# Optimization experiments

Hardware: AMD Instinct MI355X
Metric: run time of the kernel (lower is better)

The kernel has to match this reference:

```python
import jax, jax.numpy as jnp
import numpy as np

B, L, H, NH, NB = 16, 256, 64, 2, 2
HS = H // NH
MAXLEN, TIME_SPAN, ITEMNUM = 256, 256, 50000
NEG = -4294967295.0  # -2**32 + 1
EPS = 1e-8


def layernorm(x, g, b):
    m = jnp.mean(x, axis=-1, keepdims=True)
    v = jnp.mean((x - m) ** 2, axis=-1, keepdims=True)
    return g * (x - m) / jnp.sqrt(v + EPS) + b


def setup_inputs() -> dict:
    key = jax.random.key(0)
    ks = jax.random.split(key, 24)
    s = 0.02
    inp = {
        "seqs_data": jax.random.randint(ks[0], (B, L), 0, ITEMNUM, dtype=jnp.int32),
        "seqs": jax.random.normal(ks[1], (B, L, H), dtype=jnp.float32),
        "positions": jax.random.randint(ks[2], (B, L), 0, MAXLEN, dtype=jnp.int32),
        "time_matrices": jax.random.randint(ks[3], (B, L, L), 0, TIME_SPAN + 1, dtype=jnp.int32),
        "abs_pos_K_tab": jax.random.normal(ks[4], (MAXLEN, H)) * s,
        "abs_pos_V_tab": jax.random.normal(ks[5], (MAXLEN, H)) * s,
        "time_K_tab": jax.random.normal(ks[6], (TIME_SPAN + 1, H)) * s,
        "time_V_tab": jax.random.normal(ks[7], (TIME_SPAN + 1, H)) * s,
        "Qw": jax.random.normal(ks[8], (NB, H, H)) * s,
        "Qb": jnp.zeros((NB, H)),
        "Kw": jax.random.normal(ks[9], (NB, H, H)) * s,
        "Kb": jnp.zeros((NB, H)),
        "Vw": jax.random.normal(ks[10], (NB, H, H)) * s,
        "Vb": jnp.zeros((NB, H)),
        "ln1_g": jnp.ones((NB, H)), "ln1_b": jnp.zeros((NB, H)),
        "ln2_g": jnp.ones((NB, H)), "ln2_b": jnp.zeros((NB, H)),
        "ffn_W1": jax.random.normal(ks[11], (NB, H, H)) * s,
        "ffn_b1": jnp.zeros((NB, H)),
        "ffn_W2": jax.random.normal(ks[12], (NB, H, H)) * s,
        "ffn_b2": jnp.zeros((NB, H)),
        "last_g": jnp.ones((H,)), "last_b": jnp.zeros((H,)),
    }
    return inp


def _forward(seqs_data, seqs, positions, time_matrices,
             abs_pos_K_tab, abs_pos_V_tab, time_K_tab, time_V_tab,
             Qw, Qb, Kw, Kb, Vw, Vb, ln1_g, ln1_b, ln2_g, ln2_b,
             ffn_W1, ffn_b1, ffn_W2, ffn_b2, last_g, last_b):
    # abs-pos embeddings with padding_idx=0 (zero row, no grad flow to it)
    pos_keep = (positions != 0)[..., None].astype(seqs.dtype)
    abs_pos_K = abs_pos_K_tab[positions] * pos_keep            # [B,L,H]
    abs_pos_V = abs_pos_V_tab[positions] * pos_keep
    time_K = time_K_tab[time_matrices]                         # [B,L,L,H]
    time_V = time_V_tab[time_matrices]
    tmK = time_K.reshape(B, L, L, NH, HS)
    tmV = time_V.reshape(B, L, L, NH, HS)
    aK = abs_pos_K.reshape(B, L, NH, HS)
    aV = abs_pos_V.reshape(B, L, NH, HS)

    timeline_mask = (seqs_data == ITEMNUM - 1)                 # [B,L] True = pad
    keep = (~timeline_mask)[..., None].astype(seqs.dtype)
    seqs = seqs * keep
    causal = ~jnp.tril(jnp.ones((L, L), dtype=bool))           # [L,L] upper tri
    full_mask = timeline_mask[:, None, :, None] | causal[None, None]  # [B,1,L,L]

    for i in range(NB):
        q_in = layernorm(seqs, ln1_g[i], ln1_b[i])
        Q = (q_in @ Qw[i].T + Qb[i]).reshape(B, L, NH, HS)
        K = (seqs @ Kw[i].T + Kb[i]).reshape(B, L, NH, HS)
        V = (seqs @ Vw[i].T + Vb[i]).reshape(B, L, NH, HS)
        aw = (jnp.einsum('blhd,bmhd->bhlm', Q, K)
              + jnp.einsum('blhd,bmhd->bhlm', Q, aK)
              + jnp.einsum('blmhd,blhd->bhlm', tmK, Q)) / (HS ** 0.5)
        aw = jnp.where(full_mask, NEG, aw)
        A = jax.nn.softmax(aw, axis=-1)                        # [B,NH,L,L]
        out = (jnp.einsum('bhlm,bmhd->blhd', A, V)
               + jnp.einsum('bhlm,bmhd->blhd', A, aV)
               + jnp.einsum('bhlm,blmhd->blhd', A, tmV)).reshape(B, L, H)
        seqs = q_in + out
        seqs = layernorm(seqs, ln2_g[i], ln2_b[i])
        h = jax.nn.relu(seqs @ ffn_W1[i].T + ffn_b1[i])
        seqs = (h @ ffn_W2[i].T + ffn_b2[i]) + seqs
        seqs = seqs * keep
    return layernorm(seqs, last_g, last_b)


def reference(seqs_data, seqs, positions, time_matrices,
              abs_pos_K_tab, abs_pos_V_tab, time_K_tab, time_V_tab,
              Qw, Qb, Kw, Kb, Vw, Vb, ln1_g, ln1_b, ln2_g, ln2_b,
              ffn_W1, ffn_b1, ffn_W2, ffn_b2, last_g, last_b):
    return _forward(seqs_data, seqs, positions, time_matrices,
                    abs_pos_K_tab, abs_pos_V_tab, time_K_tab, time_V_tab,
                    Qw, Qb, Kw, Kb, Vw, Vb, ln1_g, ln1_b, ln2_g, ln2_b,
                    ffn_W1, ffn_b1, ffn_W2, ffn_b2, last_g, last_b)
```

## Files before the change

### kernel.cpp

```cpp
#include <hip/hip_runtime.h>
#include <math.h>

#define SEQL  256
#define HDIM  64
#define PADID 49999
#define NEGV  -4294967295.0f
#define LNEPS 1e-8f
#define INV_SQRT_HS 0.17677669529663687f
#define TKC   257
#define TKTLD 260
#define QG    4
#define ROWS  4096

struct AttnS {
    float qs[QG][HDIM];
    float Tk[QG][2][TKTLD];
    float A[QG][2][SEQL];
    float Wl[QG][2][TKTLD];
    float outred[4][QG][HDIM];
    float redm[QG][2][4];
    float reds[QG][2][4];
};
struct WorkS {
    float t0[64][65];
    float t1[64][65];
    float xs[4][HDIM];
    float qs[4][HDIM];
    float kx[HDIM][5];
};
union SmemU { AttnS a; WorkS w; };

struct FArgs {
    const int *seqs_data, *positions, *tmat;
    const float *apK, *apV, *tVtab, *tKtabT;
    const float *Qo_in, *KpT_in, *Vp_in, *q_in_in;
    const float *g2, *b2, *W1, *fb1, *W2, *fb2;
    const float *g1n, *b1n, *Qw, *Qb, *Kw, *Kb, *Vw, *Vb;
    float *q_in_out, *Qo_out, *KpT_out, *Vp_out;
    const float *lastg, *lastb;
    float *out;
    int final_ln;
};

__device__ __forceinline__ float waveReduceSum(float v) {
#pragma unroll
    for (int o = 32; o > 0; o >>= 1) v += __shfl_xor(v, o);
    return v;
}

__global__ __launch_bounds__(256, 4) void prep_kernel(
    const float* __restrict__ seqs, const int* __restrict__ seqs_data,
    const int* __restrict__ positions,
    const float* __restrict__ Qw, const float* __restrict__ Qb,
    const float* __restrict__ Kw, const float* __restrict__ Kb,
    const float* __restrict__ Vw, const float* __restrict__ Vb,
    const float* __restrict__ g1, const float* __restrict__ b1,
    const float* __restrict__ apK, const float* __restrict__ apV,
    const float* __restrict__ tKtab, float* __restrict__ tKtabT,
    float* __restrict__ q_in, float* __restrict__ Qo,
    float* __restrict__ KpT, float* __restrict__ Vp)
{
    __shared__ WorkS sw;
    const int tid = threadIdx.x;
    const int hw = blockIdx.x;
    const int blk = ((hw & 7) << 7) | (hw >> 3);
    const int w = tid >> 6, t = tid & 63;
    const int row0 = blk << 2;
    const int row = row0 + w;

    if (hw < 5) {
        const int s0 = hw * 64;
        const int nrows = (hw == 4) ? (TKC - 256) : 64;
#pragma unroll
        for (int pp = 0; pp < 16; ++pp) {
            int r = pp*4 + w;
            if (r < nrows) sw.t0[r][t] = tKtab[(size_t)(s0 + r)*64 + t];
        }
        __syncthreads();
#pragma unroll
        for (int pp = 0; pp < 16; ++pp) {
            int dd = pp*4 + w;
            if (t < nrows) tKtabT[dd*TKTLD + s0 + t] = sw.t0[t][dd];
        }
        __syncthreads();
    }

    float x = seqs[(size_t)row * HDIM + t];
    if (seqs_data[row] == PADID) x = 0.f;
    float mean = waveReduceSum(x) * (1.f / HDIM);
    float d = x - mean;
    float var = waveReduceSum(d * d) * (1.f / HDIM);
    float q = g1[t] * d / sqrtf(var + LNEPS) + b1[t];

    sw.xs[w][t] = x;
    sw.qs[w][t] = q;
    q_in[(size_t)row * HDIM + t] = q;

    int pos = positions[row];
    float aK = pos ? apK[(size_t)pos * HDIM + t] : 0.f;
    float aV = pos ? apV[(size_t)pos * HDIM + t] : 0.f;

#pragma unroll
    for (int pp = 0; pp < 16; ++pp) {
        sw.t0[pp*4 + w][t] = Qw[(size_t)(pp*4 + w)*64 + t];
        sw.t1[pp*4 + w][t] = Kw[(size_t)(pp*4 + w)*64 + t];
    }
    __syncthreads();
    float aq = 0.f, ak = 0.f;
#pragma unroll 16
    for (int mth = 0; mth < 64; ++mth) {
        aq += sw.qs[w][mth] * sw.t0[t][mth];
        ak += sw.xs[w][mth] * sw.t1[t][mth];
    }
    Qo[(size_t)row*HDIM + t] = aq + Qb[t];
    sw.kx[t][w] = ak + Kb[t] + aK;
    __syncthreads();
#pragma unroll
    for (int pp = 0; pp < 16; ++pp)
        sw.t0[pp*4 + w][t] = Vw[(size_t)(pp*4 + w)*64 + t];
    KpT[(size_t)(tid>>2)*ROWS + row0 + (tid&3)] = sw.kx[tid>>2][tid&3];
    __syncthreads();
    float av = 0.f;
#pragma unroll 16
    for (int mth = 0; mth < 64; ++mth)
        av += sw.xs[w][mth] * sw.t0[t][mth];
    Vp[(size_t)row*HDIM + t] = av + Vb[t] + aV;
}

__global__ __launch_bounds__(256, 4) void attn_ffn_kernel(FArgs p)
{
    __shared__ SmemU sm;
    __shared__ float x2s[QG][HDIM];
    const int tid = threadIdx.x;
    const int hw = blockIdx.x;
    const int blk = ((hw & 7) << 7) | (hw >> 3);
    const int b = blk >> 6, al0 = (blk & 63) << 2;
    const int row0 = blk << 2;
    const int w = tid >> 6, t = tid & 63;
    const int m = tid, lane = t, wv = w;

    for (int k = tid; k < QG*2*TKTLD; k += 256) (&sm.a.Wl[0][0][0])[k] = 0.f;
    sm.a.qs[w][t] = p.Qo_in[(size_t)(row0 + w)*HDIM + t];
    bool qpad[QG]; bool anypad = false;
#pragma unroll
    for (int li = 0; li < QG; ++li) {
        qpad[li] = (p.seqs_data[row0 + li] == PADID);
        anypad |= qpad[li];
    }
    const int lmax = al0 + QG - 1;
    int tmc[QG];
#pragma unroll
    for (int li = 0; li < QG; ++li)
        tmc[li] = p.tmat[(size_t)(row0 + li)*SEQL + m];
    __syncthreads();

    for (int c = tid; c < TKC; c += 256) {
        float a00=0,a10=0,a20=0,a30=0,a01=0,a11=0,a21=0,a31=0;
#pragma unroll 8
        for (int dd = 0; dd < 32; ++dd) {
            float tt = p.tKtabT[dd*TKTLD + c];
            a00 += tt*sm.a.qs[0][dd]; a10 += tt*sm.a.qs[1][dd];
            a20 += tt*sm.a.qs[2][dd]; a30 += tt*sm.a.qs[3][dd];
        }
#pragma unroll 8
        for (int dd = 32; dd < 64; ++dd) {
            float tt = p.tKtabT[dd*TKTLD + c];
            a01 += tt*sm.a.qs[0][dd]; a11 += tt*sm.a.qs[1][dd];
            a21 += tt*sm.a.qs[2][dd]; a31 += tt*sm.a.qs[3][dd];
        }
        sm.a.Tk[0][0][c]=a00; sm.a.Tk[1][0][c]=a10; sm.a.Tk[2][0][c]=a20; sm.a.Tk[3][0][c]=a30;
        sm.a.Tk[0][1][c]=a01; sm.a.Tk[1][1][c]=a11; sm.a.Tk[2][1][c]=a21; sm.a.Tk[3][1][c]=a31;
    }
    __syncthreads();

    float p0v[QG], p1v[QG];
    const bool waveAllMasked = (wv*64 > lmax) && !anypad;
    if (waveAllMasked) {
#pragma unroll
        for (int li = 0; li < QG; ++li) { p0v[li] = NEGV; p1v[li] = NEGV; }
    } else {
        float s0[QG] = {0,0,0,0}, s1[QG] = {0,0,0,0};
        const float* kpb = p.KpT_in + (size_t)b*SEQL + m;
#pragma unroll 8
        for (int dd = 0; dd < 32; ++dd) {
            float kv0 = kpb[(size_t)dd*ROWS];
            float kv1 = kpb[(size_t)(dd+32)*ROWS];
#pragma unroll
            for (int li = 0; li < QG; ++li) {
                s0[li] += kv0 * sm.a.qs[li][dd];
                s1[li] += kv1 * sm.a.qs[li][dd+32];
            }
        }
#pragma unroll
        for (int li = 0; li < QG; ++li) {
            float v0 = (s0[li] + sm.a.Tk[li][0][tmc[li]]) * INV_SQRT_HS;
            float v1 = (s1[li] + sm.a.Tk[li][1][tmc[li]]) * INV_SQRT_HS;
            bool masked = (m > al0 + li) || qpad[li];
            p0v[li] = masked ? NEGV : v0;
            p1v[li] = masked ? NEGV : v1;
        }
    }
#pragma unroll
    for (int li = 0; li < QG; ++li) {
        float a0 = p0v[li], a1 = p1v[li];
#pragma unroll
        for (int o = 32; o > 0; o >>= 1) {
            a0 = fmaxf(a0, __shfl_xor(a0, o));
            a1 = fmaxf(a1, __shfl_xor(a1, o));
        }
        if (lane == 0) { sm.a.redm[li][0][wv] = a0; sm.a.redm[li][1][wv] = a1; }
    }
    __syncthreads();
#pragma unroll
    for (int li = 0; li < QG; ++li) {
        float m0 = fmaxf(fmaxf(sm.a.redm[li][0][0], sm.a.redm[li][0][1]),
                         fmaxf(sm.a.redm[li][0][2], sm.a.redm[li][0][3]));
        float m1 = fmaxf(fmaxf(sm.a.redm[li][1][0], sm.a.redm[li][1][1]),
                         fmaxf(sm.a.redm[li][1][2], sm.a.redm[li][1][3]));
        float e0 = __expf(p0v[li] - m0), e1 = __expf(p1v[li] - m1);
        p0v[li] = e0; p1v[li] = e1;
        float ts0 = waveReduceSum(e0), ts1 = waveReduceSum(e1);
        if (lane == 0) { sm.a.reds[li][0][wv] = ts0; sm.a.reds[li][1][wv] = ts1; }
    }
    __syncthreads();
#pragma unroll
    for (int li = 0; li < QG; ++li) {
        float sum0 = sm.a.reds[li][0][0]+sm.a.reds[li][0][1]+sm.a.reds[li][0][2]+sm.a.reds[li][0][3];
        float sum1 = sm.a.reds[li][1][0]+sm.a.reds[li][1][1]+sm.a.reds[li][1][2]+sm.a.reds[li][1][3];
        float a0 = p0v[li]/sum0, a1 = p1v[li]/sum1;
        sm.a.A[li][0][m] = a0; sm.a.A[li][1][m] = a1;
        if (a0 != 0.f) atomicAdd(&sm.a.Wl[li][0][tmc[li]], a0);
        if (a1 != 0.f) atomicAdd(&sm.a.Wl[li][1][tmc[li]], a1);
    }
    __syncthreads();

    {
        const int hd = lane, chunk = wv, hh = hd >> 5;
        float acc0=0.f, acc1=0.f, acc2=0.f, acc3=0.f;
        const int mend = anypad ? SEQL : (lmax + 1 < SEQL ? lmax + 1 : SEQL);
        const float* vpb = p.Vp_in + (size_t)(b*SEQL)*HDIM + hd;
        int mm = chunk;
        for (; mm + 12 < mend; mm += 16) {
            float v0 = vpb[(size_t)(mm)    * HDIM];
            float v1 = vpb[(size_t)(mm+4)  * HDIM];
            float v2 = vpb[(size_t)(mm+8)  * HDIM];
            float v3 = vpb[(size_t)(mm+12) * HDIM];
            acc0 += sm.a.A[0][hh][mm]*v0 + sm.a.A[0][hh][mm+4]*v1 + sm.a.A[0][hh][mm+8]*v2 + sm.a.A[0][hh][mm+12]*v3;
            acc1 += sm.a.A[1][hh][mm]*v0 + sm.a.A[1][hh][mm+4]*v1 + sm.a.A[1][hh][mm+8]*v2 + sm.a.A[1][hh][mm+12]*v3;
            acc2 += sm.a.A[2][hh][mm]*v0 + sm.a.A[2][hh][mm+4]*v1 + sm.a.A[2][hh][mm+8]*v2 + sm.a.A[2][hh][mm+12]*v3;
            acc3 += sm.a.A[3][hh][mm]*v0 + sm.a.A[3][hh][mm+4]*v1 + sm.a.A[3][hh][mm+8]*v2 + sm.a.A[3][hh][mm+12]*v3;
        }
        for (; mm < mend; mm += 4) {
            float vp = vpb[(size_t)mm * HDIM];
            acc0 += sm.a.A[0][hh][mm]*vp; acc1 += sm.a.A[1][hh][mm]*vp;
            acc2 += sm.a.A[2][hh][mm]*vp; acc3 += sm.a.A[3][hh][mm]*vp;
        }
        const float* tvb = p.tVtab + hd;
        int c = chunk;
        for (; c + 12 < TKC; c += 16) {
            float t0 = tvb[(size_t)(c)    * HDIM];
            float t1 = tvb[(size_t)(c+4)  * HDIM];
            float t2 = tvb[(size_t)(c+8)  * HDIM];
            float t3 = tvb[(size_t)(c+12) * HDIM];
            acc0 += sm.a.Wl[0][hh][c]*t0 + sm.a.Wl[0][hh][c+4]*t1 + sm.a.Wl[0][hh][c+8]*t2 + sm.a.Wl[0][hh][c+12]*t3;
            acc1 += sm.a.Wl[1][hh][c]*t0 + sm.a.Wl[1][hh][c+4]*t1 + sm.a.Wl[1][hh][c+8]*t2 + sm.a.Wl[1][hh][c+12]*t3;
            acc2 += sm.a.Wl[2][hh][c]*t0 + sm.a.Wl[2][hh][c+4]*t1 + sm.a.Wl[2][hh][c+8]*t2 + sm.a.Wl[2][hh][c+12]*t3;
            acc3 += sm.a.Wl[3][hh][c]*t0 + sm.a.Wl[3][hh][c+4]*t1 + sm.a.Wl[3][hh][c+8]*t2 + sm.a.Wl[3][hh][c+12]*t3;
        }
        for (; c < TKC; c += 4) {
            float tv = tvb[(size_t)c * HDIM];
            acc0 += sm.a.Wl[0][hh][c]*tv; acc1 += sm.a.Wl[1][hh][c]*tv;
            acc2 += sm.a.Wl[2][hh][c]*tv; acc3 += sm.a.Wl[3][hh][c]*tv;
        }
        sm.a.outred[chunk][0][hd] = acc0;
        sm.a.outred[chunk][1][hd] = acc1;
        sm.a.outred[chunk][2][hd] = acc2;
        sm.a.outred[chunk][3][hd] = acc3;
    }
    __syncthreads();
    {
        float o = sm.a.outred[0][w][t] + sm.a.outred[1][w][t]
                + sm.a.outred[2][w][t] + sm.a.outred[3][w][t];
        x2s[w][t] = p.q_in_in[(size_t)(row0 + w)*HDIM + t] + o;
    }
    __syncthreads();

    const int row = row0 + w;
    float xv = x2s[w][t];
    float mean = waveReduceSum(xv) * (1.f/HDIM);
    float d = xv - mean;
    float var = waveReduceSum(d*d) * (1.f/HDIM);
    float s = p.g2[t] * d / sqrtf(var + LNEPS) + p.b2[t];
    sm.w.xs[w][t] = s;
#pragma unroll
    for (int pp = 0; pp < 16; ++pp) {
        sm.w.t0[pp*4 + w][t] = p.W1[(size_t)(pp*4 + w)*64 + t];
        sm.w.t1[pp*4 + w][t] = p.W2[(size_t)(pp*4 + w)*64 + t];
    }
    __syncthreads();
    float ha = 0.f;
#pragma unroll 16
    for (int mth = 0; mth < 64; ++mth) ha += sm.w.xs[w][mth] * sm.w.t0[t][mth];
    float hv = fmaxf(ha + p.fb1[t], 0.f);
    sm.w.qs[w][t] = hv;
    float ya = 0.f;
#pragma unroll 16
    for (int mth = 0; mth < 64; ++mth) ya += sm.w.qs[w][mth] * sm.w.t1[t][mth];
    float y = ya + p.fb2[t] + s;
    if (p.seqs_data[row] == PADID) y = 0.f;

    if (!p.final_ln) {
        float mean2 = waveReduceSum(y) * (1.f/HDIM);
        float d2 = y - mean2;
        float var2 = waveReduceSum(d2*d2) * (1.f/HDIM);
        float q = p.g1n[t] * d2 / sqrtf(var2 + LNEPS) + p.b1n[t];
        __syncthreads();
        sm.w.xs[w][t] = y;
        sm.w.qs[w][t] = q;
        p.q_in_out[(size_t)row*HDIM + t] = q;

        int pos = p.positions[row];
        float aK = pos ? p.apK[(size_t)pos*HDIM + t] : 0.f;
        float aV = pos ? p.apV[(size_t)pos*HDIM + t] : 0.f;
#pragma unroll
        for (int pp = 0; pp < 16; ++pp) {
            sm.w.t0[pp*4 + w][t] = p.Qw[(size_t)(pp*4 + w)*64 + t];
            sm.w.t1[pp*4 + w][t] = p.Kw[(size_t)(pp*4 + w)*64 + t];
        }
        __syncthreads();
        float aq = 0.f, ak = 0.f;
#pragma unroll 16
        for (int mth = 0; mth < 64; ++mth) {
            aq += sm.w.qs[w][mth] * sm.w.t0[t][mth];
            ak += sm.w.xs[w][mth] * sm.w.t1[t][mth];
        }
        p.Qo_out[(size_t)row*HDIM + t] = aq + p.Qb[t];
        sm.w.kx[t][w] = ak + p.Kb[t] + aK;
        __syncthreads();
#pragma unroll
        for (int pp = 0; pp < 16; ++pp)
            sm.w.t0[pp*4 + w][t] = p.Vw[(size_t)(pp*4 + w)*64 + t];
        p.KpT_out[(size_t)(tid>>2)*ROWS + row0 + (tid&3)] = sm.w.kx[tid>>2][tid&3];
        __syncthreads();
        float av = 0.f;
#pragma unroll 16
        for (int mth = 0; mth < 64; ++mth)
            av += sm.w.xs[w][mth] * sm.w.t0[t][mth];
        p.Vp_out[(size_t)row*HDIM + t] = av + p.Vb[t] + aV;
    } else {
        float m2 = waveReduceSum(y) * (1.f/HDIM);
        float dd = y - m2;
        float v2 = waveReduceSum(dd*dd) * (1.f/HDIM);
        p.out[(size_t)row*HDIM + t] = p.lastg[t] * dd / sqrtf(v2 + LNEPS) + p.lastb[t];
    }
}

extern "C" void kernel_launch(void* const* d_in, const int* in_sizes, int n_in,
                              void* d_out, int out_size, void* d_ws, size_t ws_size,
                              hipStream_t stream) {
    const int*   seqs_data = (const int*)d_in[0];
    const float* seqs      = (const float*)d_in[1];
    const int*   positions = (const int*)d_in[2];
    const int*   tmat      = (const int*)d_in[3];
    const float* apK       = (const float*)d_in[4];
    const float* apV       = (const float*)d_in[5];
    const float* tKtab     = (const float*)d_in[6];
    const float* tVtab     = (const float*)d_in[7];
    const float* Qw = (const float*)d_in[8];
    const float* Qb = (const float*)d_in[9];
    const float* Kw = (const float*)d_in[10];
    const float* Kb = (const float*)d_in[11];
    const float* Vw = (const float*)d_in[12];
    const float* Vb = (const float*)d_in[13];
    const float* g1 = (const float*)d_in[14];
    const float* b1 = (const float*)d_in[15];
    const float* g2 = (const float*)d_in[16];
    const float* b2 = (const float*)d_in[17];
    const float* W1 = (const float*)d_in[18];
    const float* fb1 = (const float*)d_in[19];
    const float* W2 = (const float*)d_in[20];
    const float* fb2 = (const float*)d_in[21];
    const float* lastg = (const float*)d_in[22];
    const float* lastb = (const float*)d_in[23];

    const size_t N = (size_t)ROWS * HDIM;
    float* ws = (float*)d_ws;
    float* q_in0 = ws + 0*N;
    float* q_in1 = ws + 1*N;
    float* Qo0   = ws + 2*N;
    float* Qo1   = ws + 3*N;
    float* Vp0   = ws + 4*N;
    float* Vp1   = ws + 5*N;
    float* KpT0  = ws + 6*N;
    float* KpT1  = ws + 7*N;
    float* tKtabT = ws + 8*N;

    prep_kernel<<<1024, 256, 0, stream>>>(
        seqs, seqs_data, positions,
        Qw, Qb, Kw, Kb, Vw, Vb, g1, b1, apK, apV,
        tKtab, tKtabT, q_in0, Qo0, KpT0, Vp0);

    FArgs a0;
    a0.seqs_data = seqs_data; a0.positions = positions; a0.tmat = tmat;
    a0.apK = apK; a0.apV = apV; a0.tVtab = tVtab; a0.tKtabT = tKtabT;
    a0.Qo_in = Qo0; a0.KpT_in = KpT0; a0.Vp_in = Vp0; a0.q_in_in = q_in0;
    a0.g2 = g2; a0.b2 = b2; a0.W1 = W1; a0.fb1 = fb1; a0.W2 = W2; a0.fb2 = fb2;
    a0.g1n = g1 + HDIM; a0.b1n = b1 + HDIM;
    a0.Qw = Qw + 4096; a0.Qb = Qb + HDIM;
    a0.Kw = Kw + 4096; a0.Kb = Kb + HDIM;
    a0.Vw = Vw + 4096; a0.Vb = Vb + HDIM;
    a0.q_in_out = q_in1; a0.Qo_out = Qo1; a0.KpT_out = KpT1; a0.Vp_out = Vp1;
    a0.lastg = lastg; a0.lastb = lastb; a0.out = (float*)d_out;
    a0.final_ln = 0;
    attn_ffn_kernel<<<1024, 256, 0, stream>>>(a0);

    FArgs a1 = a0;
    a1.Qo_in = Qo1; a1.KpT_in = KpT1; a1.Vp_in = Vp1; a1.q_in_in = q_in1;
    a1.g2 = g2 + HDIM; a1.b2 = b2 + HDIM;
    a1.W1 = W1 + 4096; a1.fb1 = fb1 + HDIM;
    a1.W2 = W2 + 4096; a1.fb2 = fb2 + HDIM;
    a1.final_ln = 1;
    attn_ffn_kernel<<<1024, 256, 0, stream>>>(a1);
}
```

Measured before the change: 213.2 us.

## Pre-transpose weights in prep kernel and read them from global to shrink LDS

```diff
diff --git a/kernel.cpp b/kernel.cpp
--- a/kernel.cpp
+++ b/kernel.cpp
@@ -13,7 +13,6 @@
 #define ROWS  4096
 
 struct AttnS {
-    float qs[QG][HDIM];
     float Tk[QG][2][TKTLD];
     float A[QG][2][SEQL];
     float Wl[QG][2][TKTLD];
@@ -21,21 +20,19 @@
     float redm[QG][2][4];
     float reds[QG][2][4];
 };
-struct WorkS {
-    float t0[64][65];
-    float t1[64][65];
+struct WorkSm {
     float xs[4][HDIM];
     float qs[4][HDIM];
     float kx[HDIM][5];
 };
-union SmemU { AttnS a; WorkS w; };
+union SmemU { AttnS a; WorkSm w; };
 
 struct FArgs {
     const int *seqs_data, *positions, *tmat;
     const float *apK, *apV, *tVtab, *tKtabT;
     const float *Qo_in, *KpT_in, *Vp_in, *q_in_in;
-    const float *g2, *b2, *W1, *fb1, *W2, *fb2;
-    const float *g1n, *b1n, *Qw, *Qb, *Kw, *Kb, *Vw, *Vb;
+    const float *g2, *b2, *W1T, *fb1, *W2T, *fb2;
+    const float *g1n, *b1n, *QwT, *Qb, *KwT, *Kb, *VwT, *Vb;
     float *q_in_out, *Qo_out, *KpT_out, *Vp_out;
     const float *lastg, *lastb;
     float *out;
@@ -56,11 +53,17 @@
     const float* __restrict__ Vw, const float* __restrict__ Vb,
     const float* __restrict__ g1, const float* __restrict__ b1,
     const float* __restrict__ apK, const float* __restrict__ apV,
-    const float* __restrict__ tKtab, float* __restrict__ tKtabT,
+    const float* __restrict__ tKtab, const float* __restrict__ W1,
+    const float* __restrict__ W2,
+    float* __restrict__ tKtabT, float* __restrict__ WT,
     float* __restrict__ q_in, float* __restrict__ Qo,
     float* __restrict__ KpT, float* __restrict__ Vp)
 {
-    __shared__ WorkS sw;
+    __shared__ float t0[64][65];
+    __shared__ float t1[64][65];
+    __shared__ float xs[4][HDIM];
+    __shared__ float qs[4][HDIM];
+    __shared__ float kx[HDIM][5];
     const int tid = threadIdx.x;
     const int hw = blockIdx.x;
     const int blk = ((hw & 7) << 7) | (hw >> 3);
@@ -74,14 +77,28 @@
 #pragma unroll
         for (int pp = 0; pp < 16; ++pp) {
             int r = pp*4 + w;
-            if (r < nrows) sw.t0[r][t] = tKtab[(size_t)(s0 + r)*64 + t];
+            if (r < nrows) t0[r][t] = tKtab[(size_t)(s0 + r)*64 + t];
         }
         __syncthreads();
 #pragma unroll
         for (int pp = 0; pp < 16; ++pp) {
             int dd = pp*4 + w;
-            if (t < nrows) tKtabT[dd*TKTLD + s0 + t] = sw.t0[t][dd];
-        }
+            if (t < nrows) tKtabT[dd*TKTLD + s0 + t] = t0[t][dd];
+        }
+        __syncthreads();
+    } else if (hw < 12) {
+        const int wi = hw - 5;
+        const float* src = (wi == 0) ? W1 : (wi == 1) ? W2 :
+                           (wi == 2) ? Qw + 4096 : (wi == 3) ? Kw + 4096 :
+                           (wi == 4) ? Vw + 4096 : (wi == 5) ? W1 + 4096 : W2 + 4096;
+        float* dst = WT + (size_t)wi * 4096;
+#pragma unroll
+        for (int pp = 0; pp < 16; ++pp)
+            t0[pp*4 + w][t] = src[(size_t)(pp*4 + w)*64 + t];
+        __syncthreads();
+#pragma unroll
+        for (int pp = 0; pp < 16; ++pp)
+            dst[(size_t)(pp*4 + w)*64 + t] = t0[t][pp*4 + w];
         __syncthreads();
     }
 
@@ -92,8 +109,8 @@
     float var = waveReduceSum(d * d) * (1.f / HDIM);
     float q = g1[t] * d / sqrtf(var + LNEPS) + b1[t];
 
-    sw.xs[w][t] = x;
-    sw.qs[w][t] = q;
+    xs[w][t] = x;
+    qs[w][t] = q;
     q_in[(size_t)row * HDIM + t] = q;
 
     int pos = positions[row];
@@ -102,32 +119,32 @@
 
 #pragma unroll
     for (int pp = 0; pp < 16; ++pp) {
-        sw.t0[pp*4 + w][t] = Qw[(size_t)(pp*4 + w)*64 + t];
-        sw.t1[pp*4 + w][t] = Kw[(size_t)(pp*4 + w)*64 + t];
+        t0[pp*4 + w][t] = Qw[(size_t)(pp*4 + w)*64 + t];
+        t1[pp*4 + w][t] = Kw[(size_t)(pp*4 + w)*64 + t];
     }
     __syncthreads();
     float aq = 0.f, ak = 0.f;
 #pragma unroll 16
     for (int mth = 0; mth < 64; ++mth) {
-        aq += sw.qs[w][mth] * sw.t0[t][mth];
-        ak += sw.xs[w][mth] * sw.t1[t][mth];
+        aq += qs[w][mth] * t0[t][mth];
+        ak += xs[w][mth] * t1[t][mth];
     }
     Qo[(size_t)row*HDIM + t] = aq + Qb[t];
-    sw.kx[t][w] = ak + Kb[t] + aK;
+    kx[t][w] = ak + Kb[t] + aK;
     __syncthreads();
 #pragma unroll
     for (int pp = 0; pp < 16; ++pp)
-        sw.t0[pp*4 + w][t] = Vw[(size_t)(pp*4 + w)*64 + t];
-    KpT[(size_t)(tid>>2)*ROWS + row0 + (tid&3)] = sw.kx[tid>>2][tid&3];
+        t0[pp*4 + w][t] = Vw[(size_t)(pp*4 + w)*64 + t];
+    KpT[(size_t)(tid>>2)*ROWS + row0 + (tid&3)] = kx[tid>>2][tid&3];
     __syncthreads();
     float av = 0.f;
 #pragma unroll 16
     for (int mth = 0; mth < 64; ++mth)
-        av += sw.xs[w][mth] * sw.t0[t][mth];
+        av += xs[w][mth] * t0[t][mth];
     Vp[(size_t)row*HDIM + t] = av + Vb[t] + aV;
 }
 
-__global__ __launch_bounds__(256, 4) void attn_ffn_kernel(FArgs p)
+__global__ __launch_bounds__(256, 5) void attn_ffn_kernel(FArgs p)
 {
     __shared__ SmemU sm;
     __shared__ float x2s[QG][HDIM];
@@ -140,7 +157,6 @@
     const int m = tid, lane = t, wv = w;
 
     for (int k = tid; k < QG*2*TKTLD; k += 256) (&sm.a.Wl[0][0][0])[k] = 0.f;
-    sm.a.qs[w][t] = p.Qo_in[(size_t)(row0 + w)*HDIM + t];
     bool qpad[QG]; bool anypad = false;
 #pragma unroll
     for (int li = 0; li < QG; ++li) {
@@ -152,24 +168,29 @@
 #pragma unroll
     for (int li = 0; li < QG; ++li)
         tmc[li] = p.tmat[(size_t)(row0 + li)*SEQL + m];
-    __syncthreads();
-
-    for (int c = tid; c < TKC; c += 256) {
-        float a00=0,a10=0,a20=0,a30=0,a01=0,a11=0,a21=0,a31=0;
+
+    {
+        const float* q0 = p.Qo_in + (size_t)(row0+0)*HDIM;
+        const float* q1 = p.Qo_in + (size_t)(row0+1)*HDIM;
+        const float* q2 = p.Qo_in + (size_t)(row0+2)*HDIM;
+        const float* q3 = p.Qo_in + (size_t)(row0+3)*HDIM;
+        for (int c = tid; c < TKC; c += 256) {
+            float a00=0,a10=0,a20=0,a30=0,a01=0,a11=0,a21=0,a31=0;
 #pragma unroll 8
-        for (int dd = 0; dd < 32; ++dd) {
-            float tt = p.tKtabT[dd*TKTLD + c];
-            a00 += tt*sm.a.qs[0][dd]; a10 += tt*sm.a.qs[1][dd];
-            a20 += tt*sm.a.qs[2][dd]; a30 += tt*sm.a.qs[3][dd];
-        }
+            for (int dd = 0; dd < 32; ++dd) {
+                float tt = p.tKtabT[dd*TKTLD + c];
+                a00 += tt*q0[dd]; a10 += tt*q1[dd];
+                a20 += tt*q2[dd]; a30 += tt*q3[dd];
+            }
 #pragma unroll 8
-        for (int dd = 32; dd < 64; ++dd) {
-            float tt = p.tKtabT[dd*TKTLD + c];
-            a01 += tt*sm.a.qs[0][dd]; a11 += tt*sm.a.qs[1][dd];
-            a21 += tt*sm.a.qs[2][dd]; a31 += tt*sm.a.qs[3][dd];
-        }
-        sm.a.Tk[0][0][c]=a00; sm.a.Tk[1][0][c]=a10; sm.a.Tk[2][0][c]=a20; sm.a.Tk[3][0][c]=a30;
-        sm.a.Tk[0][1][c]=a01; sm.a.Tk[1][1][c]=a11; sm.a.Tk[2][1][c]=a21; sm.a.Tk[3][1][c]=a31;
+            for (int dd = 32; dd < 64; ++dd) {
+                float tt = p.tKtabT[dd*TKTLD + c];
+                a01 += tt*q0[dd]; a11 += tt*q1[dd];
+                a21 += tt*q2[dd]; a31 += tt*q3[dd];
+            }
+            sm.a.Tk[0][0][c]=a00; sm.a.Tk[1][0][c]=a10; sm.a.Tk[2][0][c]=a20; sm.a.Tk[3][0][c]=a30;
+            sm.a.Tk[0][1][c]=a01; sm.a.Tk[1][1][c]=a11; sm.a.Tk[2][1][c]=a21; sm.a.Tk[3][1][c]=a31;
+        }
     }
     __syncthreads();
 
@@ -181,14 +202,15 @@
     } else {
         float s0[QG] = {0,0,0,0}, s1[QG] = {0,0,0,0};
         const float* kpb = p.KpT_in + (size_t)b*SEQL + m;
+        const float* qq = p.Qo_in + (size_t)row0*HDIM;
 #pragma unroll 8
         for (int dd = 0; dd < 32; ++dd) {
             float kv0 = kpb[(size_t)dd*ROWS];
             float kv1 = kpb[(size_t)(dd+32)*ROWS];
 #pragma unroll
             for (int li = 0; li < QG; ++li) {
-                s0[li] += kv0 * sm.a.qs[li][dd];
-                s1[li] += kv1 * sm.a.qs[li][dd+32];
+                s0[li] += kv0 * qq[li*HDIM + dd];
+                s1[li] += kv1 * qq[li*HDIM + dd + 32];
             }
         }
 #pragma unroll
@@ -292,20 +314,16 @@
     float var = waveReduceSum(d*d) * (1.f/HDIM);
     float s = p.g2[t] * d / sqrtf(var + LNEPS) + p.b2[t];
     sm.w.xs[w][t] = s;
-#pragma unroll
-    for (int pp = 0; pp < 16; ++pp) {
-        sm.w.t0[pp*4 + w][t] = p.W1[(size_t)(pp*4 + w)*64 + t];
-        sm.w.t1[pp*4 + w][t] = p.W2[(size_t)(pp*4 + w)*64 + t];
-    }
-    __syncthreads();
     float ha = 0.f;
 #pragma unroll 16
-    for (int mth = 0; mth < 64; ++mth) ha += sm.w.xs[w][mth] * sm.w.t0[t][mth];
+    for (int mth = 0; mth < 64; ++mth)
+        ha += sm.w.xs[w][mth] * p.W1T[(size_t)mth*64 + t];
     float hv = fmaxf(ha + p.fb1[t], 0.f);
     sm.w.qs[w][t] = hv;
     float ya = 0.f;
 #pragma unroll 16
-    for (int mth = 0; mth < 64; ++mth) ya += sm.w.qs[w][mth] * sm.w.t1[t][mth];
+    for (int mth = 0; mth < 64; ++mth)
+        ya += sm.w.qs[w][mth] * p.W2T[(size_t)mth*64 + t];
     float y = ya + p.fb2[t] + s;
     if (p.seqs_data[row] == PADID) y = 0.f;
 
@@ -314,7 +332,6 @@
         float d2 = y - mean2;
         float var2 = waveReduceSum(d2*d2) * (1.f/HDIM);
         float q = p.g1n[t] * d2 / sqrtf(var2 + LNEPS) + p.b1n[t];
-        __syncthreads();
         sm.w.xs[w][t] = y;
         sm.w.qs[w][t] = q;
         p.q_in_out[(size_t)row*HDIM + t] = q;
@@ -322,31 +339,19 @@
         int pos = p.positions[row];
         float aK = pos ? p.apK[(size_t)pos*HDIM + t] : 0.f;
         float aV = pos ? p.apV[(size_t)pos*HDIM + t] : 0.f;
-#pragma unroll
-        for (int pp = 0; pp < 16; ++pp) {
-            sm.w.t0[pp*4 + w][t] = p.Qw[(size_t)(pp*4 + w)*64 + t];
-            sm.w.t1[pp*4 + w][t] = p.Kw[(size_t)(pp*4 + w)*64 + t];
-        }
-        __syncthreads();
-        float aq = 0.f, ak = 0.f;
+        float aq = 0.f, ak = 0.f, av = 0.f;
 #pragma unroll 16
         for (int mth = 0; mth < 64; ++mth) {
-            aq += sm.w.qs[w][mth] * sm.w.t0[t][mth];
-            ak += sm.w.xs[w][mth] * sm.w.t1[t][mth];
+            float qm = sm.w.qs[w][mth], ym = sm.w.xs[w][mth];
+            aq += qm * p.QwT[(size_t)mth*64 + t];
+            ak += ym * p.KwT[(size_t)mth*64 + t];
+            av += ym * p.VwT[(size_t)mth*64 + t];
         }
         p.Qo_out[(size_t)row*HDIM + t] = aq + p.Qb[t];
+        p.Vp_out[(size_t)row*HDIM + t] = av + p.Vb[t] + aV;
         sm.w.kx[t][w] = ak + p.Kb[t] + aK;
         __syncthreads();
-#pragma unroll
-        for (int pp = 0; pp < 16; ++pp)
-            sm.w.t0[pp*4 + w][t] = p.Vw[(size_t)(pp*4 + w)*64 + t];
         p.KpT_out[(size_t)(tid>>2)*ROWS + row0 + (tid&3)] = sm.w.kx[tid>>2][tid&3];
-        __syncthreads();
-        float av = 0.f;
-#pragma unroll 16
-        for (int mth = 0; mth < 64; ++mth)
-            av += sm.w.xs[w][mth] * sm.w.t0[t][mth];
-        p.Vp_out[(size_t)row*HDIM + t] = av + p.Vb[t] + aV;
     } else {
         float m2 = waveReduceSum(y) * (1.f/HDIM);
         float dd = y - m2;
@@ -394,21 +399,25 @@
     float* KpT0  = ws + 6*N;
     float* KpT1  = ws + 7*N;
     float* tKtabT = ws + 8*N;
+    float* WT    = tKtabT + 64*TKTLD;
 
     prep_kernel<<<1024, 256, 0, stream>>>(
         seqs, seqs_data, positions,
         Qw, Qb, Kw, Kb, Vw, Vb, g1, b1, apK, apV,
-        tKtab, tKtabT, q_in0, Qo0, KpT0, Vp0);
+        tKtab, W1, W2, tKtabT, WT,
+        q_in0, Qo0, KpT0, Vp0);
 
     FArgs a0;
     a0.seqs_data = seqs_data; a0.positions = positions; a0.tmat = tmat;
     a0.apK = apK; a0.apV = apV; a0.tVtab = tVtab; a0.tKtabT = tKtabT;
     a0.Qo_in = Qo0; a0.KpT_in = KpT0; a0.Vp_in = Vp0; a0.q_in_in = q_in0;
-    a0.g2 = g2; a0.b2 = b2; a0.W1 = W1; a0.fb1 = fb1; a0.W2 = W2; a0.fb2 = fb2;
+    a0.g2 = g2; a0.b2 = b2;
+    a0.W1T = WT + 0*4096; a0.fb1 = fb1;
+    a0.W2T = WT + 1*4096; a0.fb2 = fb2;
     a0.g1n = g1 + HDIM; a0.b1n = b1 + HDIM;
-    a0.Qw = Qw + 4096; a0.Qb = Qb + HDIM;
-    a0.Kw = Kw + 4096; a0.Kb = Kb + HDIM;
-    a0.Vw = Vw + 4096; a0.Vb = Vb + HDIM;
+    a0.QwT = WT + 2*4096; a0.Qb = Qb + HDIM;
+    a0.KwT = WT + 3*4096; a0.Kb = Kb + HDIM;
+    a0.VwT = WT + 4*4096; a0.Vb = Vb + HDIM;
     a0.q_in_out = q_in1; a0.Qo_out = Qo1; a0.KpT_out = KpT1; a0.Vp_out = Vp1;
     a0.lastg = lastg; a0.lastb = lastb; a0.out = (float*)d_out;
     a0.final_ln = 0;
@@ -417,8 +426,8 @@
     FArgs a1 = a0;
     a1.Qo_in = Qo1; a1.KpT_in = KpT1; a1.Vp_in = Vp1; a1.q_in_in = q_in1;
     a1.g2 = g2 + HDIM; a1.b2 = b2 + HDIM;
-    a1.W1 = W1 + 4096; a1.fb1 = fb1 + HDIM;
-    a1.W2 = W2 + 4096; a1.fb2 = fb2 + HDIM;
+    a1.W1T = WT + 5*4096; a1.fb1 = fb1 + HDIM;
+    a1.W2T = WT + 6*4096; a1.fb2 = fb2 + HDIM;
     a1.final_ln = 1;
     attn_ffn_kernel<<<1024, 256, 0, stream>>>(a1);
 }
```

Result: slower. 237.7 us (+11.5%).
